# Kernel tuning notes

Measured on AMD Instinct MI355X. Metric: run time of the kernel, lower is better.

The kernel has to match this reference:

```python
import jax, jax.numpy as jnp
import numpy as np

N_NODES = 50000
N_EDGES = 800000
D_IN = 128
D_OUT = 64
E_DIM = 2
NEG_SLOPE = 0.01  # torch F.leaky_relu default


def setup_inputs() -> dict:
    key = jax.random.key(0)
    ks = jax.random.split(key, 10)
    h = jax.random.normal(ks[0], (N_NODES, D_IN), dtype=jnp.float32)
    e = jax.random.normal(ks[1], (N_EDGES, E_DIM), dtype=jnp.float32)
    src = jax.random.randint(ks[2], (N_EDGES,), 0, N_NODES, dtype=jnp.int32)
    dst = jax.random.randint(ks[3], (N_EDGES,), 0, N_NODES, dtype=jnp.int32)
    # learned params (xavier-normal-ish scaling)
    def xn(k, shape):
        fan_in, fan_out = shape[-1], shape[0]
        std = math_gain * (2.0 / (fan_in + fan_out)) ** 0.5
        return std * jax.random.normal(k, shape, dtype=jnp.float32)
    global math_gain
    math_gain = 2.0 ** 0.5  # relu gain
    W_fc = xn(ks[4], (D_OUT, D_IN))
    W_attn = xn(ks[5], (1, 2 * D_OUT + E_DIM))
    W_eatt = xn(ks[6], (E_DIM, E_DIM))
    W_e2n = xn(ks[7], (D_OUT, E_DIM))
    W_edge = xn(ks[8], (D_OUT, E_DIM))
    attn_edge = xn(ks[9], (1, 1, D_OUT))
    return {"h": h, "e": e, "src": src, "dst": dst, "W_fc": W_fc,
            "W_attn": W_attn, "W_eatt": W_eatt, "W_e2n": W_e2n,
            "W_edge": W_edge, "attn_edge": attn_edge}


def reference(h, e, src, dst, W_fc, W_attn, W_eatt, W_e2n, W_edge, attn_edge):
    n = h.shape[0]
    z = h @ W_fc.T                       # [N, Dout]
    ex = e @ W_eatt.T                    # [E, Edim]
    # edge attention logit
    feat_edge = ex @ W_edge.T            # [E, Dout]
    ee = jnp.sum(feat_edge * attn_edge.reshape(1, -1), axis=-1, keepdims=True)  # [E,1]
    z2 = jnp.concatenate([z[src], z[dst], ex], axis=1)  # [E, 2*Dout+Edim]
    a = z2 @ W_attn.T + ee               # [E, 1]
    logit = jax.nn.leaky_relu(a[:, 0], NEG_SLOPE)  # [E]
    ez = ex @ W_e2n.T                    # [E, Dout]
    # segment softmax over incoming edges per destination node
    m = jax.ops.segment_max(logit, dst, num_segments=n)
    w = jnp.exp(logit - m[dst])
    s = jax.ops.segment_sum(w, dst, num_segments=n)
    attn = w / s[dst]                    # [E]
    msg = attn[:, None] * (z[src] + ez)  # [E, Dout]
    h_out = jax.ops.segment_sum(msg, dst, num_segments=n)  # [N, Dout]
    return h_out
```

## Files before the change

### kernel.cpp

```cpp
#include <hip/hip_runtime.h>

#define D_IN 128
#define D_OUT 64
#define SCAN_B 512
#define DEG_STRIDE 16

__device__ __forceinline__ unsigned int pack_bf16x2(float a, float b) {
    unsigned int ua = __float_as_uint(a);
    unsigned int ub = __float_as_uint(b);
    ua = (ua + 0x7fffu + ((ua >> 16) & 1u)) >> 16;
    ub = (ub + 0x7fffu + ((ub >> 16) & 1u)) >> 16;
    return ua | (ub << 16);
}

__global__ __launch_bounds__(256) void fat_kernel(
    const float* __restrict__ h, const float* __restrict__ W_fc,
    const float* __restrict__ W_attn, unsigned short* __restrict__ zb,
    float* __restrict__ as_, float* __restrict__ ad_,
    const int* __restrict__ dst, int* __restrict__ deg, int* __restrict__ rank,
    const float* __restrict__ W_eatt, const float* __restrict__ W_e2n,
    const float* __restrict__ W_edge, const float* __restrict__ attn_edge,
    float* __restrict__ M0buf, float* __restrict__ M1buf, float* __restrict__ cbuf,
    int N, int E, int gemmBlocks) {
    __shared__ float As[64][68];
    __shared__ float Bs[64][64];
    int bid = blockIdx.x;
    int t = threadIdx.x;
    if (bid < gemmBlocks) {
        int n0 = bid * 64;
        int tx = t & 15, ty = t >> 4;
        float acc[4][4] = {};
#pragma unroll
        for (int kh = 0; kh < 2; ++kh) {
            int kq = kh * 16;
            for (int idx = t; idx < 1024; idx += 256) {
                int r = idx >> 4, q = idx & 15;
                float4 v = make_float4(0.f, 0.f, 0.f, 0.f);
                if (n0 + r < N) v = ((const float4*)h)[(size_t)(n0 + r) * 32 + kq + q];
                *(float4*)&As[r][q * 4] = v;
            }
            for (int idx = t; idx < 1024; idx += 256) {
                int r = idx >> 4, q = idx & 15;
                float4 v = ((const float4*)W_fc)[r * 32 + kq + q];
                *(float4*)&Bs[r][(q ^ ((r >> 2) & 15)) * 4] = v;
            }
            __syncthreads();
#pragma unroll 2
            for (int k = 0; k < 64; k += 4) {
                int bq = (((k >> 2) ^ (tx & 15))) * 4;
                float4 a[4], b[4];
#pragma unroll
                for (int i = 0; i < 4; ++i) a[i] = *(const float4*)&As[ty * 4 + i][k];
#pragma unroll
                for (int j = 0; j < 4; ++j) b[j] = *(const float4*)&Bs[tx * 4 + j][bq];
#pragma unroll
                for (int i = 0; i < 4; ++i)
#pragma unroll
                    for (int j = 0; j < 4; ++j) {
                        acc[i][j] = fmaf(a[i].x, b[j].x, acc[i][j]);
                        acc[i][j] = fmaf(a[i].y, b[j].y, acc[i][j]);
                        acc[i][j] = fmaf(a[i].z, b[j].z, acc[i][j]);
                        acc[i][j] = fmaf(a[i].w, b[j].w, acc[i][j]);
                    }
            }
            __syncthreads();
        }
        float wa[4], wb[4];
#pragma unroll
        for (int j = 0; j < 4; ++j) {
            wa[j] = W_attn[tx * 4 + j];
            wb[j] = W_attn[64 + tx * 4 + j];
        }
#pragma unroll
        for (int i = 0; i < 4; ++i) {
            int n = n0 + ty * 4 + i;
            if (n >= N) break;
            uint2 zp;
            zp.x = pack_bf16x2(acc[i][0], acc[i][1]);
            zp.y = pack_bf16x2(acc[i][2], acc[i][3]);
            ((uint2*)(zb + (size_t)n * D_OUT))[tx] = zp;
            float pa = acc[i][0] * wa[0] + acc[i][1] * wa[1] + acc[i][2] * wa[2] + acc[i][3] * wa[3];
            float pb = acc[i][0] * wb[0] + acc[i][1] * wb[1] + acc[i][2] * wb[2] + acc[i][3] * wb[3];
            for (int off = 8; off; off >>= 1) {
                pa += __shfl_xor(pa, off);
                pb += __shfl_xor(pb, off);
            }
            if (tx == 0) {
                as_[n] = pa;
                ad_[n] = pb;
            }
        }
    } else {
        int hb = bid - gemmBlocks;
        if (hb == 0 && t < 64) {
            int d = t;
            M0buf[d] = W_e2n[d * 2 + 0] * W_eatt[0] + W_e2n[d * 2 + 1] * W_eatt[2];
            M1buf[d] = W_e2n[d * 2 + 0] * W_eatt[1] + W_e2n[d * 2 + 1] * W_eatt[3];
            float p0 = W_edge[d * 2 + 0] * attn_edge[d];
            float p1 = W_edge[d * 2 + 1] * attn_edge[d];
            for (int off = 32; off; off >>= 1) {
                p0 += __shfl_xor(p0, off);
                p1 += __shfl_xor(p1, off);
            }
            if (d == 0) {
                float t0 = W_attn[128] + p0;
                float t1 = W_attn[129] + p1;
                cbuf[0] = W_eatt[0] * t0 + W_eatt[2] * t1;
                cbuf[1] = W_eatt[1] * t0 + W_eatt[3] * t1;
            }
        }
        int i = hb * 256 + t;
        if (i < E) rank[i] = atomicAdd(&deg[(size_t)dst[i] * DEG_STRIDE], 1);
    }
}

__global__ void scan_kernel(const int* __restrict__ deg, int* __restrict__ row_start,
                            unsigned int* __restrict__ agg, int* __restrict__ ticket_ctr,
                            int nb, int N, int E) {
    __shared__ int wsum[8];
    __shared__ int sticket;
    __shared__ int spref;
    int t = threadIdx.x;
    if (t == 0) sticket = atomicAdd(ticket_ctr, 1);
    __syncthreads();
    int b = sticket;
    int i = b * SCAN_B + t;
    int v = (i < N) ? deg[(size_t)i * DEG_STRIDE] : 0;
    int lane = t & 63, w = t >> 6;
    int sc = v;
    for (int off = 1; off < 64; off <<= 1) {
        int x = __shfl_up(sc, off);
        if (lane >= off) sc += x;
    }
    if (lane == 63) wsum[w] = sc;
    __syncthreads();
    if (w == 0 && lane < 8) {
        int x = wsum[lane];
        for (int off = 1; off < 8; off <<= 1) {
            int y = __shfl_up(x, off);
            if (lane >= off) x += y;
        }
        wsum[lane] = x;
    }
    __syncthreads();
    int wofs = (w > 0) ? wsum[w - 1] : 0;
    int incl = wofs + sc;
    if (t == SCAN_B - 1)
        __hip_atomic_store(&agg[b], 0x80000000u | (unsigned)incl, __ATOMIC_RELEASE,
                           __HIP_MEMORY_SCOPE_AGENT);
    if (t < 64) {
        int accp = 0;
        for (int j = t; j < b; j += 64) {
            unsigned x;
            do {
                x = __hip_atomic_load(&agg[j], __ATOMIC_ACQUIRE, __HIP_MEMORY_SCOPE_AGENT);
            } while (!(x & 0x80000000u));
            accp += (int)(x & 0x7fffffffu);
        }
        for (int off = 32; off; off >>= 1) accp += __shfl_xor(accp, off);
        if (t == 0) spref = accp;
    }
    __syncthreads();
    if (i < N) row_start[i] = spref + incl - v;
    if (b == 0 && t == 0) row_start[N] = E;
}

__global__ void build_logit_kernel(const float* __restrict__ e,
                                   const int* __restrict__ src,
                                   const int* __restrict__ dst,
                                   const float* __restrict__ as_,
                                   const float* __restrict__ ad_,
                                   const float* __restrict__ cbuf,
                                   const int* __restrict__ row_start,
                                   const int* __restrict__ rank,
                                   float4* __restrict__ pay, int E) {
    int i = blockIdx.x * 256 + threadIdx.x;
    if (i >= E) return;
    int si = src[i], di = dst[i];
    float2 ev = ((const float2*)e)[i];
    float a = as_[si] + ad_[di] + ev.x * cbuf[0] + ev.y * cbuf[1];
    float lg = a > 0.f ? a : 0.01f * a;
    float w = __expf(lg);
    int pos = row_start[di] + rank[i];
    pay[pos] = make_float4(w, __int_as_float(si), ev.x, ev.y);
}

__global__ __launch_bounds__(256) void fused_kernel(const unsigned short* __restrict__ zb,
                                                    const float4* __restrict__ pay,
                                                    const int* __restrict__ row_start,
                                                    const float* __restrict__ M0buf,
                                                    const float* __restrict__ M1buf,
                                                    float* __restrict__ hout, int N) {
    int wv = threadIdx.x >> 6, l = threadIdx.x & 63;
    int n = blockIdx.x * 4 + wv;
    if (n >= N) return;
    int start = row_start[n], end = row_start[n + 1];
    int g = l >> 3, q = l & 7;
    float* orow = &hout[(size_t)n * D_OUT + q * 8];
    if (start == end) {
        if (g == 0) {
            *(float4*)orow = make_float4(0.f, 0.f, 0.f, 0.f);
            *(float4*)(orow + 4) = make_float4(0.f, 0.f, 0.f, 0.f);
        }
        return;
    }
    float accv[8] = {};
    float s = 0.f, s0 = 0.f, s1 = 0.f;
    for (int base = start; base < end; base += 64) {
        int j = base + l;
        float w = 0.f, e0 = 0.f, e1 = 0.f;
        int sj = 0;
        if (j < end) {
            float4 P = pay[j];
            w = P.x;
            sj = __float_as_int(P.y);
            e0 = P.z;
            e1 = P.w;
        }
        s += w;
        s0 = fmaf(w, e0, s0);
        s1 = fmaf(w, e1, s1);
        int cnt = end - base;
        if (cnt > 64) cnt = 64;
        int iters = (cnt + 7) >> 3;
        for (int jj = 0; jj < iters; ++jj) {
            int srcl = jj * 8 + g;
            float wb = __shfl(w, srcl);
            int sb = __shfl(sj, srcl);
            uint4 zv = *(const uint4*)((const char*)zb + ((size_t)sb << 7) + (q << 4));
#pragma unroll
            for (int k = 0; k < 4; ++k) {
                unsigned int u = (&zv.x)[k];
                float lo = __uint_as_float(u << 16);
                float hi = __uint_as_float(u & 0xffff0000u);
                accv[2 * k] = fmaf(wb, lo, accv[2 * k]);
                accv[2 * k + 1] = fmaf(wb, hi, accv[2 * k + 1]);
            }
        }
    }
#pragma unroll
    for (int off = 8; off <= 32; off <<= 1) {
#pragma unroll
        for (int k = 0; k < 8; ++k) accv[k] += __shfl_xor(accv[k], off);
    }
    for (int off = 32; off; off >>= 1) {
        s += __shfl_xor(s, off);
        s0 += __shfl_xor(s0, off);
        s1 += __shfl_xor(s1, off);
    }
    if (g == 0) {
        float inv = 1.f / s;
        float o[8];
#pragma unroll
        for (int k = 0; k < 8; ++k) {
            float m0 = M0buf[q * 8 + k];
            float m1 = M1buf[q * 8 + k];
            o[k] = (accv[k] + m0 * s0 + m1 * s1) * inv;
        }
        *(float4*)orow = make_float4(o[0], o[1], o[2], o[3]);
        *(float4*)(orow + 4) = make_float4(o[4], o[5], o[6], o[7]);
    }
}

extern "C" void kernel_launch(void* const* d_in, const int* in_sizes, int n_in,
                              void* d_out, int out_size, void* d_ws, size_t ws_size,
                              hipStream_t stream) {
    const float* h = (const float*)d_in[0];
    const float* e = (const float*)d_in[1];
    const int* src = (const int*)d_in[2];
    const int* dst = (const int*)d_in[3];
    const float* W_fc = (const float*)d_in[4];
    const float* W_attn = (const float*)d_in[5];
    const float* W_eatt = (const float*)d_in[6];
    const float* W_e2n = (const float*)d_in[7];
    const float* W_edge = (const float*)d_in[8];
    const float* attn_edge = (const float*)d_in[9];
    float* hout = (float*)d_out;

    const int N = in_sizes[0] / D_IN;
    const int E = in_sizes[2];
    const int nb = (N + SCAN_B - 1) / SCAN_B;
    const int gemmBlocks = (N + 63) / 64;
    const int histBlocks = (E + 255) / 256;

    float4* pay = (float4*)d_ws;
    unsigned short* zb = (unsigned short*)(pay + E);
    float* as_ = (float*)(zb + (size_t)N * 64);
    float* ad_ = as_ + N;
    float* M0buf = ad_ + N;
    float* M1buf = M0buf + 64;
    float* cbuf = M1buf + 64;
    int* deg = (int*)(cbuf + 2);
    unsigned int* agg = (unsigned int*)(deg + (size_t)N * DEG_STRIDE);
    int* ticket_ctr = (int*)(agg + 128);
    int* rank = ticket_ctr + 1;
    int* row_start = rank + E;

    (void)hipMemsetAsync(deg, 0, ((size_t)N * DEG_STRIDE + 129) * sizeof(int), stream);
    fat_kernel<<<gemmBlocks + histBlocks, 256, 0, stream>>>(
        h, W_fc, W_attn, zb, as_, ad_, dst, deg, rank,
        W_eatt, W_e2n, W_edge, attn_edge, M0buf, M1buf, cbuf, N, E, gemmBlocks);
    scan_kernel<<<nb, SCAN_B, 0, stream>>>(deg, row_start, agg, ticket_ctr, nb, N, E);
    build_logit_kernel<<<(E + 255) / 256, 256, 0, stream>>>(e, src, dst, as_, ad_, cbuf,
                                                            row_start, rank, pay, E);
    fused_kernel<<<(N + 3) / 4, 256, 0, stream>>>(zb, pay, row_start, M0buf, M1buf, hout, N);
}
```

Before: 104.3 us.

## Merge scan, logit build and aggregation into one cooperative persistent kernel

```diff
diff --git a/kernel.cpp b/kernel.cpp
--- a/kernel.cpp
+++ b/kernel.cpp
@@ -1,8 +1,10 @@
 #include <hip/hip_runtime.h>
+#include <hip/hip_cooperative_groups.h>
+
+namespace cg = cooperative_groups;
 
 #define D_IN 128
 #define D_OUT 64
-#define SCAN_B 512
 #define DEG_STRIDE 16
 
 __device__ __forceinline__ unsigned int pack_bf16x2(float a, float b) {
@@ -114,151 +116,147 @@
     }
 }
 
-__global__ void scan_kernel(const int* __restrict__ deg, int* __restrict__ row_start,
-                            unsigned int* __restrict__ agg, int* __restrict__ ticket_ctr,
-                            int nb, int N, int E) {
-    __shared__ int wsum[8];
-    __shared__ int sticket;
+__global__ void tail_kernel(const int* __restrict__ deg, int* __restrict__ row_start,
+                            unsigned int* __restrict__ agg,
+                            const float* __restrict__ e, const int* __restrict__ src,
+                            const int* __restrict__ dst, const float* __restrict__ as_,
+                            const float* __restrict__ ad_, const float* __restrict__ cbuf,
+                            const int* __restrict__ rank, float4* __restrict__ pay,
+                            const unsigned short* __restrict__ zb,
+                            const float* __restrict__ M0buf, const float* __restrict__ M1buf,
+                            float* __restrict__ hout, int nb, int N, int E) {
+    cg::grid_group grid = cg::this_grid();
+    __shared__ int wsum[4];
     __shared__ int spref;
     int t = threadIdx.x;
-    if (t == 0) sticket = atomicAdd(ticket_ctr, 1);
-    __syncthreads();
-    int b = sticket;
-    int i = b * SCAN_B + t;
-    int v = (i < N) ? deg[(size_t)i * DEG_STRIDE] : 0;
-    int lane = t & 63, w = t >> 6;
-    int sc = v;
-    for (int off = 1; off < 64; off <<= 1) {
-        int x = __shfl_up(sc, off);
-        if (lane >= off) sc += x;
+    int b = blockIdx.x;
+
+    if (b < nb) {
+        int i = b * 256 + t;
+        int v = (i < N) ? deg[(size_t)i * DEG_STRIDE] : 0;
+        int lane = t & 63, w = t >> 6;
+        int sc = v;
+        for (int off = 1; off < 64; off <<= 1) {
+            int x = __shfl_up(sc, off);
+            if (lane >= off) sc += x;
+        }
+        if (lane == 63) wsum[w] = sc;
+        __syncthreads();
+        if (w == 0 && lane < 4) {
+            int x = wsum[lane];
+            for (int off = 1; off < 4; off <<= 1) {
+                int y = __shfl_up(x, off);
+                if (lane >= off) x += y;
+            }
+            wsum[lane] = x;
+        }
+        __syncthreads();
+        int wofs = (w > 0) ? wsum[w - 1] : 0;
+        int incl = wofs + sc;
+        if (t == 255)
+            __hip_atomic_store(&agg[b], 0x80000000u | (unsigned)incl, __ATOMIC_RELEASE,
+                               __HIP_MEMORY_SCOPE_AGENT);
+        if (t < 64) {
+            int accp = 0;
+            for (int j = t; j < b; j += 64) {
+                unsigned x;
+                do {
+                    x = __hip_atomic_load(&agg[j], __ATOMIC_ACQUIRE,
+                                          __HIP_MEMORY_SCOPE_AGENT);
+                } while (!(x & 0x80000000u));
+                accp += (int)(x & 0x7fffffffu);
+            }
+            for (int off = 32; off; off >>= 1) accp += __shfl_xor(accp, off);
+            if (t == 0) spref = accp;
+        }
+        __syncthreads();
+        if (i < N) row_start[i] = spref + incl - v;
+        if (b == 0 && t == 0) row_start[N] = E;
     }
-    if (lane == 63) wsum[w] = sc;
-    __syncthreads();
-    if (w == 0 && lane < 8) {
-        int x = wsum[lane];
-        for (int off = 1; off < 8; off <<= 1) {
-            int y = __shfl_up(x, off);
-            if (lane >= off) x += y;
-        }
-        wsum[lane] = x;
+    grid.sync();
+
+    for (int i = b * 256 + t; i < E; i += gridDim.x * 256) {
+        int si = src[i], di = dst[i];
+        float2 ev = ((const float2*)e)[i];
+        float a = as_[si] + ad_[di] + ev.x * cbuf[0] + ev.y * cbuf[1];
+        float lg = a > 0.f ? a : 0.01f * a;
+        float w = __expf(lg);
+        int pos = row_start[di] + rank[i];
+        pay[pos] = make_float4(w, __int_as_float(si), ev.x, ev.y);
     }
-    __syncthreads();
-    int wofs = (w > 0) ? wsum[w - 1] : 0;
-    int incl = wofs + sc;
-    if (t == SCAN_B - 1)
-        __hip_atomic_store(&agg[b], 0x80000000u | (unsigned)incl, __ATOMIC_RELEASE,
-                           __HIP_MEMORY_SCOPE_AGENT);
-    if (t < 64) {
-        int accp = 0;
-        for (int j = t; j < b; j += 64) {
-            unsigned x;
-            do {
-                x = __hip_atomic_load(&agg[j], __ATOMIC_ACQUIRE, __HIP_MEMORY_SCOPE_AGENT);
-            } while (!(x & 0x80000000u));
-            accp += (int)(x & 0x7fffffffu);
-        }
-        for (int off = 32; off; off >>= 1) accp += __shfl_xor(accp, off);
-        if (t == 0) spref = accp;
-    }
-    __syncthreads();
-    if (i < N) row_start[i] = spref + incl - v;
-    if (b == 0 && t == 0) row_start[N] = E;
-}
-
-__global__ void build_logit_kernel(const float* __restrict__ e,
-                                   const int* __restrict__ src,
-                                   const int* __restrict__ dst,
-                                   const float* __restrict__ as_,
-                                   const float* __restrict__ ad_,
-                                   const float* __restrict__ cbuf,
-                                   const int* __restrict__ row_start,
-                                   const int* __restrict__ rank,
-                                   float4* __restrict__ pay, int E) {
-    int i = blockIdx.x * 256 + threadIdx.x;
-    if (i >= E) return;
-    int si = src[i], di = dst[i];
-    float2 ev = ((const float2*)e)[i];
-    float a = as_[si] + ad_[di] + ev.x * cbuf[0] + ev.y * cbuf[1];
-    float lg = a > 0.f ? a : 0.01f * a;
-    float w = __expf(lg);
-    int pos = row_start[di] + rank[i];
-    pay[pos] = make_float4(w, __int_as_float(si), ev.x, ev.y);
-}
-
-__global__ __launch_bounds__(256) void fused_kernel(const unsigned short* __restrict__ zb,
-                                                    const float4* __restrict__ pay,
-                                                    const int* __restrict__ row_start,
-                                                    const float* __restrict__ M0buf,
-                                                    const float* __restrict__ M1buf,
-                                                    float* __restrict__ hout, int N) {
-    int wv = threadIdx.x >> 6, l = threadIdx.x & 63;
-    int n = blockIdx.x * 4 + wv;
-    if (n >= N) return;
-    int start = row_start[n], end = row_start[n + 1];
+    grid.sync();
+
+    int wv = t >> 6, l = t & 63;
     int g = l >> 3, q = l & 7;
-    float* orow = &hout[(size_t)n * D_OUT + q * 8];
-    if (start == end) {
+    int nblk = (N + 3) >> 2;
+    for (int vb = b; vb < nblk; vb += gridDim.x) {
+        int n = vb * 4 + wv;
+        if (n >= N) continue;
+        int start = row_start[n], end = row_start[n + 1];
+        float* orow = &hout[(size_t)n * D_OUT + q * 8];
+        if (start == end) {
+            if (g == 0) {
+                *(float4*)orow = make_float4(0.f, 0.f, 0.f, 0.f);
+                *(float4*)(orow + 4) = make_float4(0.f, 0.f, 0.f, 0.f);
+            }
+            continue;
+        }
+        float accv[8] = {};
+        float s = 0.f, s0 = 0.f, s1 = 0.f;
+        for (int base = start; base < end; base += 64) {
+            int j = base + l;
+            float w = 0.f, e0 = 0.f, e1 = 0.f;
+            int sj = 0;
+            if (j < end) {
+                float4 P = pay[j];
+                w = P.x;
+                sj = __float_as_int(P.y);
+                e0 = P.z;
+                e1 = P.w;
+            }
+            s += w;
+            s0 = fmaf(w, e0, s0);
+            s1 = fmaf(w, e1, s1);
+            int cnt = end - base;
+            if (cnt > 64) cnt = 64;
+            int iters = (cnt + 7) >> 3;
+            for (int jj = 0; jj < iters; ++jj) {
+                int srcl = jj * 8 + g;
+                float wb = __shfl(w, srcl);
+                int sb = __shfl(sj, srcl);
+                uint4 zv = *(const uint4*)((const char*)zb + ((size_t)sb << 7) + (q << 4));
+#pragma unroll
+                for (int k = 0; k < 4; ++k) {
+                    unsigned int u = (&zv.x)[k];
+                    float lo = __uint_as_float(u << 16);
+                    float hi = __uint_as_float(u & 0xffff0000u);
+                    accv[2 * k] = fmaf(wb, lo, accv[2 * k]);
+                    accv[2 * k + 1] = fmaf(wb, hi, accv[2 * k + 1]);
+                }
+            }
+        }
+#pragma unroll
+        for (int off = 8; off <= 32; off <<= 1) {
+#pragma unroll
+            for (int k = 0; k < 8; ++k) accv[k] += __shfl_xor(accv[k], off);
+        }
+        for (int off = 32; off; off >>= 1) {
+            s += __shfl_xor(s, off);
+            s0 += __shfl_xor(s0, off);
+            s1 += __shfl_xor(s1, off);
+        }
         if (g == 0) {
-            *(float4*)orow = make_float4(0.f, 0.f, 0.f, 0.f);
-            *(float4*)(orow + 4) = make_float4(0.f, 0.f, 0.f, 0.f);
-        }
-        return;
-    }
-    float accv[8] = {};
-    float s = 0.f, s0 = 0.f, s1 = 0.f;
-    for (int base = start; base < end; base += 64) {
-        int j = base + l;
-        float w = 0.f, e0 = 0.f, e1 = 0.f;
-        int sj = 0;
-        if (j < end) {
-            float4 P = pay[j];
-            w = P.x;
-            sj = __float_as_int(P.y);
-            e0 = P.z;
-            e1 = P.w;
-        }
-        s += w;
-        s0 = fmaf(w, e0, s0);
-        s1 = fmaf(w, e1, s1);
-        int cnt = end - base;
-        if (cnt > 64) cnt = 64;
-        int iters = (cnt + 7) >> 3;
-        for (int jj = 0; jj < iters; ++jj) {
-            int srcl = jj * 8 + g;
-            float wb = __shfl(w, srcl);
-            int sb = __shfl(sj, srcl);
-            uint4 zv = *(const uint4*)((const char*)zb + ((size_t)sb << 7) + (q << 4));
-#pragma unroll
-            for (int k = 0; k < 4; ++k) {
-                unsigned int u = (&zv.x)[k];
-                float lo = __uint_as_float(u << 16);
-                float hi = __uint_as_float(u & 0xffff0000u);
-                accv[2 * k] = fmaf(wb, lo, accv[2 * k]);
-                accv[2 * k + 1] = fmaf(wb, hi, accv[2 * k + 1]);
-            }
-        }
-    }
-#pragma unroll
-    for (int off = 8; off <= 32; off <<= 1) {
-#pragma unroll
-        for (int k = 0; k < 8; ++k) accv[k] += __shfl_xor(accv[k], off);
-    }
-    for (int off = 32; off; off >>= 1) {
-        s += __shfl_xor(s, off);
-        s0 += __shfl_xor(s0, off);
-        s1 += __shfl_xor(s1, off);
-    }
-    if (g == 0) {
-        float inv = 1.f / s;
-        float o[8];
-#pragma unroll
-        for (int k = 0; k < 8; ++k) {
-            float m0 = M0buf[q * 8 + k];
-            float m1 = M1buf[q * 8 + k];
-            o[k] = (accv[k] + m0 * s0 + m1 * s1) * inv;
-        }
-        *(float4*)orow = make_float4(o[0], o[1], o[2], o[3]);
-        *(float4*)(orow + 4) = make_float4(o[4], o[5], o[6], o[7]);
+            float inv = 1.f / s;
+            float o[8];
+#pragma unroll
+            for (int k = 0; k < 8; ++k) {
+                float m0 = M0buf[q * 8 + k];
+                float m1 = M1buf[q * 8 + k];
+                o[k] = (accv[k] + m0 * s0 + m1 * s1) * inv;
+            }
+            *(float4*)orow = make_float4(o[0], o[1], o[2], o[3]);
+            *(float4*)(orow + 4) = make_float4(o[4], o[5], o[6], o[7]);
+        }
     }
 }
 
@@ -279,7 +277,7 @@
 
     const int N = in_sizes[0] / D_IN;
     const int E = in_sizes[2];
-    const int nb = (N + SCAN_B - 1) / SCAN_B;
+    const int nb = (N + 255) / 256;
     const int gemmBlocks = (N + 63) / 64;
     const int histBlocks = (E + 255) / 256;
 
@@ -292,16 +290,24 @@
     float* cbuf = M1buf + 64;
     int* deg = (int*)(cbuf + 2);
     unsigned int* agg = (unsigned int*)(deg + (size_t)N * DEG_STRIDE);
-    int* ticket_ctr = (int*)(agg + 128);
-    int* rank = ticket_ctr + 1;
+    int* rank = (int*)(agg + 256);
     int* row_start = rank + E;
 
-    (void)hipMemsetAsync(deg, 0, ((size_t)N * DEG_STRIDE + 129) * sizeof(int), stream);
+    (void)hipMemsetAsync(deg, 0, ((size_t)N * DEG_STRIDE + 256) * sizeof(int), stream);
     fat_kernel<<<gemmBlocks + histBlocks, 256, 0, stream>>>(
         h, W_fc, W_attn, zb, as_, ad_, dst, deg, rank,
         W_eatt, W_e2n, W_edge, attn_edge, M0buf, M1buf, cbuf, N, E, gemmBlocks);
-    scan_kernel<<<nb, SCAN_B, 0, stream>>>(deg, row_start, agg, ticket_ctr, nb, N, E);
-    build_logit_kernel<<<(E + 255) / 256, 256, 0, stream>>>(e, src, dst, as_, ad_, cbuf,
-                                                            row_start, rank, pay, E);
-    fused_kernel<<<(N + 3) / 4, 256, 0, stream>>>(zb, pay, row_start, M0buf, M1buf, hout, N);
+
+    int blocksPerCU = 0;
+    (void)hipOccupancyMaxActiveBlocksPerMultiprocessor(&blocksPerCU,
+                                                       (const void*)tail_kernel, 256, 0);
+    if (blocksPerCU < 1) blocksPerCU = 1;
+    int grid = blocksPerCU * 256;
+    void* args[] = {(void*)&deg, (void*)&row_start, (void*)&agg, (void*)&e,
+                    (void*)&src, (void*)&dst, (void*)&as_, (void*)&ad_,
+                    (void*)&cbuf, (void*)&rank, (void*)&pay, (void*)&zb,
+                    (void*)&M0buf, (void*)&M1buf, (void*)&hout,
+                    (void*)&nb, (void*)&N, (void*)&E};
+    (void)hipLaunchCooperativeKernel((const void*)tail_kernel, dim3(grid), dim3(256),
+                                     args, 0, stream);
 }
```

Result: slower. 396.6 us (+280.0%).
